# Kernel tuning notes

Measured on AMD Instinct MI355X. Metric: run time of the kernel, lower is better.

Reference implementation:

```python
import jax, jax.numpy as jnp
import numpy as np

N_NODES = 100_000
N_EDGES = 3_200_000
D_IN, D_EDGE, D_HID, D_OUT = 8, 4, 32, 16
NEG_SLOPE = 0.2  # PyG GATv2Conv default


def setup_inputs() -> dict:
    key = jax.random.key(0)
    ks = jax.random.split(key, 13)
    s = 0.1
    return {
        "x": jax.random.normal(ks[0], (N_NODES, D_IN), jnp.float32),
        "edge_index": jax.random.randint(ks[1], (2, N_EDGES), 0, N_NODES, dtype=jnp.int64),
        "edge_attr": jax.random.normal(ks[2], (N_EDGES, D_EDGE), jnp.float32),
        "Wl1": jax.random.normal(ks[3], (D_IN, D_HID), jnp.float32) * s,
        "Wr1": jax.random.normal(ks[4], (D_IN, D_HID), jnp.float32) * s,
        "We1": jax.random.normal(ks[5], (D_EDGE, D_HID), jnp.float32) * s,
        "att1": jax.random.normal(ks[6], (D_HID,), jnp.float32) * s,
        "b1": jnp.zeros((D_HID,), jnp.float32),
        "Wl2": jax.random.normal(ks[7], (D_HID, D_OUT), jnp.float32) * s,
        "Wr2": jax.random.normal(ks[8], (D_HID, D_OUT), jnp.float32) * s,
        "We2": jax.random.normal(ks[9], (D_EDGE, D_OUT), jnp.float32) * s,
        "att2": jax.random.normal(ks[10], (D_OUT,), jnp.float32) * s,
        "b2": jnp.zeros((D_OUT,), jnp.float32),
    }


def _segment_softmax(score, seg, n):
    m = jax.ops.segment_max(score, seg, num_segments=n)
    e = jnp.exp(score - m[seg])
    z = jax.ops.segment_sum(e, seg, num_segments=n)
    return e / z[seg]


def _gatv2(x, src, dst, ea_raw, Wl, Wr, We, att, bias, n):
    # GATv2 (heads=1): score_ij = att . leaky_relu(Wl x_j + Wr x_i + We e_ij)
    xl = x @ Wl            # [N, d]
    xr = x @ Wr            # [N, d]
    ea = ea_raw @ We       # [E, d]
    h = jax.nn.leaky_relu(xl[src] + xr[dst] + ea, NEG_SLOPE)  # [E, d]
    score = h @ att        # [E]
    alpha = _segment_softmax(score, dst, n)
    out = jax.ops.segment_sum(alpha[:, None] * xl[src], dst, num_segments=n)
    return out + bias


def reference(x, edge_index, edge_attr, Wl1, Wr1, We1, att1, b1, Wl2, Wr2, We2, att2, b2):
    n = x.shape[0]
    src, dst = edge_index[0], edge_index[1]
    # add_self_loops=True with fill_value='mean': self-loop edge_attr = mean of
    # incoming raw edge_attr per target node (0 for isolated targets)
    ones = jnp.ones((src.shape[0],), x.dtype)
    cnt = jax.ops.segment_sum(ones, dst, num_segments=n)
    loop_attr = jax.ops.segment_sum(edge_attr, dst, num_segments=n) / jnp.maximum(cnt, 1.0)[:, None]
    ar = jnp.arange(n, dtype=src.dtype)
    src2 = jnp.concatenate([src, ar])
    dst2 = jnp.concatenate([dst, ar])
    ea2 = jnp.concatenate([edge_attr, loop_attr], axis=0)
    h = jax.nn.relu(_gatv2(x, src2, dst2, ea2, Wl1, Wr1, We1, att1, b1, n))
    out = _gatv2(h, src2, dst2, ea2, Wl2, Wr2, We2, att2, b2, n)
    return out.reshape(-1)
```

## Files before the change

kernel.cpp:

```cpp
#include <hip/hip_runtime.h>

#define NEG_SLOPE 0.2f
#define CHUNK 4096
#define KMAX  512
#define NBLKMAX 1024
#define CAPB  9472

__global__ __launch_bounds__(1024) void k_bin(const int* __restrict__ ei,
                                              const float* __restrict__ eattr,
                                              int* __restrict__ cloff,
                                              int* __restrict__ ssrc,
                                              float4* __restrict__ seat,
                                              int E, int K) {
    __shared__ int s_off[KMAX + 1];
    __shared__ int s_scan[1024];
    __shared__ int s_ssrc[CHUNK];
    __shared__ float4 s_seat[CHUNK];
    int t = threadIdx.x;
    for (int i = t; i <= K; i += 1024) s_off[i] = 0;
    __syncthreads();
    int base = blockIdx.x * CHUNK;
    int Ec = min(CHUNK, E - base);
    unsigned pack[CHUNK / 1024];
#pragma unroll
    for (int i = 0; i < CHUNK / 1024; i++) {
        int el = t + 1024 * i;
        pack[i] = 0xFFFFFFFFu;
        if (el < Ec) {
            int dst = ei[E + base + el];
            int b = dst >> 8;
            int r = atomicAdd(&s_off[b], 1);
            pack[i] = ((unsigned)b << 20) | ((unsigned)(dst & 255) << 12) | (unsigned)r;
        }
    }
    __syncthreads();
    int x0 = (t <= K) ? s_off[t] : 0;
    s_scan[t] = x0;
    __syncthreads();
    for (int off = 1; off < 1024; off <<= 1) {
        int y = (t >= off) ? s_scan[t - off] : 0;
        __syncthreads();
        s_scan[t] += y;
        __syncthreads();
    }
    if (t <= K) s_off[t] = s_scan[t] - x0;
    __syncthreads();
#pragma unroll
    for (int i = 0; i < CHUNK / 1024; i++) {
        int el = t + 1024 * i;
        if (el < Ec) {
            unsigned p = pack[i];
            int b = p >> 20;
            int dl = (p >> 12) & 255;
            int r = p & 0xFFF;
            int pos = s_off[b] + r;
            int e = base + el;
            s_ssrc[pos] = ei[e] | (dl << 17);
            s_seat[pos] = *(const float4*)(eattr + 4ll * e);
        }
    }
    __syncthreads();
    for (int pos = t; pos < Ec; pos += 1024) {
        ssrc[base + pos] = s_ssrc[pos];
        seat[base + pos] = s_seat[pos];
    }
    for (int i = t; i <= K; i += 1024)
        cloff[(long long)blockIdx.x * (K + 1) + i] = s_off[i];
}

__global__ void k_transp(const int* __restrict__ in, int* __restrict__ out, int R, int C) {
    __shared__ int tile[32][33];
    int c0 = blockIdx.x * 32, r0 = blockIdx.y * 32;
    int c = c0 + threadIdx.x, r = r0 + threadIdx.y;
    if (r < R && c < C) tile[threadIdx.y][threadIdx.x] = in[(long long)r * C + c];
    __syncthreads();
    int oc = r0 + threadIdx.x, orr = c0 + threadIdx.y;
    if (orr < C && oc < R) out[(long long)orr * R + oc] = tile[threadIdx.x][threadIdx.y];
}

__global__ void k_btot(const int* __restrict__ cloffT, int* __restrict__ bucketTotal,
                       int K, int NBLK) {
    int b = (blockIdx.x * blockDim.x + threadIdx.x) >> 6;
    int lane = threadIdx.x & 63;
    if (b >= K) return;
    const int* r0 = cloffT + (long long)b * NBLK;
    const int* r1 = r0 + NBLK;
    int s = 0;
    for (int c = lane; c < NBLK; c += 64) s += r1[c] - r0[c];
#pragma unroll
    for (int off = 32; off >= 1; off >>= 1) s += __shfl_xor(s, off, 64);
    if (lane == 0) bucketTotal[b] = s;
}

__global__ void k_scanK(const int* __restrict__ bucketTotal, int* __restrict__ slotBase,
                        int* __restrict__ qofs, int N, int K) {
    __shared__ int s[512];
    int t = threadIdx.x;
    int v[4];
    int sum = 0;
    int base = t * 4;
    for (int j = 0; j < 4; j++) {
        int b = base + j, x = 0;
        if (b < K) { int nb = min(256, N - (b << 8)); x = bucketTotal[b] + nb; }
        v[j] = sum;
        sum += x;
    }
    s[t] = sum;
    __syncthreads();
    for (int off = 1; off < 512; off <<= 1) {
        int x = (t >= off) ? s[t - off] : 0;
        __syncthreads();
        s[t] += x;
        __syncthreads();
    }
    int tb = s[t] - sum;
    for (int j = 0; j < 4; j++) {
        int b = base + j;
        if (b < K) slotBase[b] = tb + v[j];
    }
    if (t == 511) { slotBase[K] = s[511]; qofs[4ll * N] = s[511]; }
}

__global__ __launch_bounds__(1024, 2) void k_perm(const int* __restrict__ ssrc,
                                                  const float4* __restrict__ seat,
                                                  const int* __restrict__ cloffT,
                                                  const int* __restrict__ slotBase,
                                                  int* __restrict__ qofs,
                                                  int* __restrict__ fsrc,
                                                  float4* __restrict__ feat,
                                                  int N, int K, int NBLK, int QDIV) {
    __shared__ int co[NBLKMAX], qq[NBLKMAX + 1], sc[NBLKMAX];
    __shared__ int hist2[1024], cur2[1024], lst2[1024], sc2[1024];
    __shared__ int hist[256];
    __shared__ float lsum[256][4];
    __shared__ int s_inv[CAPB];
    int b = blockIdx.x, t = threadIdx.x;
    int nb = min(256, N - (b << 8));
    hist2[t] = 0; cur2[t] = 0;
    if (t < 256) { lsum[t][0] = 0.f; lsum[t][1] = 0.f; lsum[t][2] = 0.f; lsum[t][3] = 0.f; }
    const int* r0 = cloffT + (long long)b * NBLK;
    const int* r1 = r0 + NBLK;
    int len = 0;
    if (t < NBLK) { int c0v = r0[t]; len = r1[t] - c0v; co[t] = c0v; }
    sc[t] = (t < NBLK) ? len : 0;
    __syncthreads();
    for (int off = 1; off < NBLKMAX; off <<= 1) {
        int x = (t >= off) ? sc[t - off] : 0;
        __syncthreads();
        sc[t] += x;
        __syncthreads();
    }
    if (t < NBLK) qq[t] = sc[t] - len;
    if (t == NBLKMAX - 1) qq[NBLK] = sc[NBLKMAX - 1];
    __syncthreads();
    int Eb = qq[NBLK];
    for (int i = t; i < Eb; i += 1024) {
        int lo2 = 0, hi2 = NBLK;
        while (lo2 + 1 < hi2) { int mid = (lo2 + hi2) >> 1; if (qq[mid] <= i) lo2 = mid; else hi2 = mid; }
        int g = lo2 * CHUNK + co[lo2] + (i - qq[lo2]);
        int p = ssrc[g];
        int q = (int)((unsigned)(p & 0x1FFFF) / (unsigned)QDIV);
        atomicAdd(&hist2[(((p >> 17) & 255) << 2) | q], 1);
    }
    __syncthreads();
    if (t < 256) {
        int c = hist2[4 * t] + hist2[4 * t + 1] + hist2[4 * t + 2] + hist2[4 * t + 3];
        hist[t] = c;
        if (t < nb) {
            int node = (b << 8) + t;
            int qs = (int)((unsigned)node / (unsigned)QDIV);
            hist2[4 * t + qs] += 1;
            cur2[4 * t + qs] = 1;
        }
    }
    __syncthreads();
    sc2[t] = hist2[t];
    __syncthreads();
    for (int off = 1; off < 1024; off <<= 1) {
        int x = (t >= off) ? sc2[t - off] : 0;
        __syncthreads();
        sc2[t] += x;
        __syncthreads();
    }
    lst2[t] = sc2[t] - hist2[t];
    __syncthreads();
    int lo = slotBase[b];
    if (t < 4 * nb) qofs[((long long)b << 10) + t] = lo + lst2[t];
    if (t < nb) {
        int node = (b << 8) + t;
        int qs = (int)((unsigned)node / (unsigned)QDIV);
        s_inv[lst2[4 * t + qs]] = -(t + 1);
    }
    __syncthreads();
    for (int i = t; i < Eb; i += 1024) {
        int lo2 = 0, hi2 = NBLK;
        while (lo2 + 1 < hi2) { int mid = (lo2 + hi2) >> 1; if (qq[mid] <= i) lo2 = mid; else hi2 = mid; }
        int g = lo2 * CHUNK + co[lo2] + (i - qq[lo2]);
        int p = ssrc[g];
        int q = (int)((unsigned)(p & 0x1FFFF) / (unsigned)QDIV);
        int bin = (((p >> 17) & 255) << 2) | q;
        int r = atomicAdd(&cur2[bin], 1);
        s_inv[lst2[bin] + r] = g;
    }
    __syncthreads();
    int tot = Eb + nb;
    int pos = t;
    for (; pos + 1024 < tot; pos += 2048) {
        int gA = s_inv[pos];
        int gB = s_inv[pos + 1024];
        bool vA = gA >= 0, vB = gB >= 0;
        int cA = vA ? gA : 0, cB = vB ? gB : 0;
        int pA = ssrc[cA];
        int pB = ssrc[cB];
        float4 aA = seat[cA];
        float4 aB = seat[cB];
        if (vA) {
            long long gp = lo + pos;
            fsrc[gp] = pA & 0x1FFFF;
            feat[gp] = aA;
            int dl = (pA >> 17) & 255;
            atomicAdd(&lsum[dl][0], aA.x); atomicAdd(&lsum[dl][1], aA.y);
            atomicAdd(&lsum[dl][2], aA.z); atomicAdd(&lsum[dl][3], aA.w);
        }
        if (vB) {
            long long gp = lo + pos + 1024;
            fsrc[gp] = pB & 0x1FFFF;
            feat[gp] = aB;
            int dl = (pB >> 17) & 255;
            atomicAdd(&lsum[dl][0], aB.x); atomicAdd(&lsum[dl][1], aB.y);
            atomicAdd(&lsum[dl][2], aB.z); atomicAdd(&lsum[dl][3], aB.w);
        }
    }
    for (; pos < tot; pos += 1024) {
        int g = s_inv[pos];
        if (g >= 0) {
            int p = ssrc[g];
            float4 a = seat[g];
            long long gp = lo + pos;
            fsrc[gp] = p & 0x1FFFF;
            feat[gp] = a;
            int dl = (p >> 17) & 255;
            atomicAdd(&lsum[dl][0], a.x); atomicAdd(&lsum[dl][1], a.y);
            atomicAdd(&lsum[dl][2], a.z); atomicAdd(&lsum[dl][3], a.w);
        }
    }
    __syncthreads();
    if (t < nb) {
        int node = (b << 8) + t;
        int qs = (int)((unsigned)node / (unsigned)QDIV);
        float inv = 1.f / fmaxf((float)hist[t], 1.f);
        long long pos2 = lo + lst2[4 * t + qs];
        fsrc[pos2] = node;
        feat[pos2] = make_float4(lsum[t][0] * inv, lsum[t][1] * inv,
                                 lsum[t][2] * inv, lsum[t][3] * inv);
    }
}

template <int DIN, int D>
__global__ void k_xform(const float* __restrict__ x, const float* __restrict__ Wl,
                        const float* __restrict__ Wr, float* __restrict__ xl,
                        float* __restrict__ xr, int N) {
    __shared__ float sWl[DIN * D], sWr[DIN * D];
    for (int i = threadIdx.x; i < DIN * D; i += blockDim.x) { sWl[i] = Wl[i]; sWr[i] = Wr[i]; }
    __syncthreads();
    int t = blockIdx.x * blockDim.x + threadIdx.x;
    if (t >= N * D) return;
    int n = t / D, d = t % D;
    const float* xp = x + (long long)n * DIN;
    float sl = 0.f, sr = 0.f;
#pragma unroll
    for (int k = 0; k < DIN; k++) {
        float xv = xp[k];
        sl += xv * sWl[k * D + d];
        sr += xv * sWr[k * D + d];
    }
    xl[t] = sl;
    xr[t] = sr;
}

template <int L>
__device__ __forceinline__ void gat_edge(bool valid, const float4& a, const float4& xlv,
                                         const float4& we0, const float4& we1,
                                         const float4& we2, const float4& we3,
                                         const float4& av, const float4& xrv,
                                         float4& acc, float& z) {
    float4 v;
    v.x = fmaf(a.x, we0.x, xrv.x); v.x = fmaf(a.y, we1.x, v.x);
    v.x = fmaf(a.z, we2.x, v.x);   v.x = fmaf(a.w, we3.x, v.x); v.x += xlv.x;
    v.y = fmaf(a.x, we0.y, xrv.y); v.y = fmaf(a.y, we1.y, v.y);
    v.y = fmaf(a.z, we2.y, v.y);   v.y = fmaf(a.w, we3.y, v.y); v.y += xlv.y;
    v.z = fmaf(a.x, we0.z, xrv.z); v.z = fmaf(a.y, we1.z, v.z);
    v.z = fmaf(a.z, we2.z, v.z);   v.z = fmaf(a.w, we3.z, v.z); v.z += xlv.z;
    v.w = fmaf(a.x, we0.w, xrv.w); v.w = fmaf(a.y, we1.w, v.w);
    v.w = fmaf(a.z, we2.w, v.w);   v.w = fmaf(a.w, we3.w, v.w); v.w += xlv.w;
    v.x = v.x > 0.f ? v.x : NEG_SLOPE * v.x;
    v.y = v.y > 0.f ? v.y : NEG_SLOPE * v.y;
    v.z = v.z > 0.f ? v.z : NEG_SLOPE * v.z;
    v.w = v.w > 0.f ? v.w : NEG_SLOPE * v.w;
    float sc = av.x * v.x + av.y * v.y + av.z * v.z + av.w * v.w;
#pragma unroll
    for (int off = L / 2; off >= 1; off >>= 1) sc += __shfl_xor(sc, off, 64);
    float ev = valid ? __expf(sc) : 0.f;
    z += ev;
    acc.x = fmaf(ev, xlv.x, acc.x);
    acc.y = fmaf(ev, xlv.y, acc.y);
    acc.z = fmaf(ev, xlv.z, acc.z);
    acc.w = fmaf(ev, xlv.w, acc.w);
}

template <int D, bool RELU>
__global__ void k_gat(const int* __restrict__ fsrc,
                      const float4* __restrict__ feat,
                      const int* __restrict__ qofs,
                      const float* __restrict__ xl, const float* __restrict__ xr,
                      const float* __restrict__ We, const float* __restrict__ att,
                      const float* __restrict__ bias, float* __restrict__ out, int N) {
    constexpr int L = D / 4;
    constexpr int G = 64 / L;
    int w = (blockIdx.x * blockDim.x + threadIdx.x) >> 6;
    int lane = threadIdx.x & 63;
    if (w >= N) return;
    int g = lane / L;
    int j = lane % L;
    int s0 = qofs[4 * w], s1 = qofs[4 * w + 4];
    int cnt = s1 - s0;

    const float4 we0 = *(const float4*)(We + 0 * D + 4 * j);
    const float4 we1 = *(const float4*)(We + 1 * D + 4 * j);
    const float4 we2 = *(const float4*)(We + 2 * D + 4 * j);
    const float4 we3 = *(const float4*)(We + 3 * D + 4 * j);
    const float4 av  = *(const float4*)(att + 4 * j);
    const float4 xrv = *(const float4*)(xr + (long long)w * D + 4 * j);

    float4 acc = make_float4(0.f, 0.f, 0.f, 0.f);
    float z = 0.f;

    int it = 0;
    for (; (it + 2) * G <= cnt; it += 2) {
        int sl = s0 + it * G + g;
        int srcA = fsrc[sl];
        int srcB = fsrc[sl + G];
        float4 aA = feat[sl];
        float4 aB = feat[sl + G];
        float4 xA = *(const float4*)(xl + (long long)srcA * D + 4 * j);
        float4 xB = *(const float4*)(xl + (long long)srcB * D + 4 * j);
        gat_edge<L>(true, aA, xA, we0, we1, we2, we3, av, xrv, acc, z);
        gat_edge<L>(true, aB, xB, we0, we1, we2, we3, av, xrv, acc, z);
    }
    for (; it * G < cnt; ++it) {
        int o = it * G + g;
        bool v = o < cnt;
        int sl = s0 + min(o, cnt - 1);
        int src = fsrc[sl];
        float4 a = feat[sl];
        float4 xv = *(const float4*)(xl + (long long)src * D + 4 * j);
        gat_edge<L>(v, a, xv, we0, we1, we2, we3, av, xrv, acc, z);
    }

#pragma unroll
    for (int off = 32; off >= L; off >>= 1) {
        acc.x += __shfl_xor(acc.x, off, 64);
        acc.y += __shfl_xor(acc.y, off, 64);
        acc.z += __shfl_xor(acc.z, off, 64);
        acc.w += __shfl_xor(acc.w, off, 64);
        z += __shfl_xor(z, off, 64);
    }

    if (g == 0) {
        float inv = 1.0f / z;
        float4 bv = *(const float4*)(bias + 4 * j);
        float4 o;
        o.x = acc.x * inv + bv.x;
        o.y = acc.y * inv + bv.y;
        o.z = acc.z * inv + bv.z;
        o.w = acc.w * inv + bv.w;
        if (RELU) {
            o.x = fmaxf(o.x, 0.f); o.y = fmaxf(o.y, 0.f);
            o.z = fmaxf(o.z, 0.f); o.w = fmaxf(o.w, 0.f);
        }
        *(float4*)(out + (long long)w * D + 4 * j) = o;
    }
}

extern "C" void kernel_launch(void* const* d_in, const int* in_sizes, int n_in,
                              void* d_out, int out_size, void* d_ws, size_t ws_size,
                              hipStream_t stream) {
    const float* x     = (const float*)d_in[0];
    const int*   ei    = (const int*)d_in[1];
    const float* eattr = (const float*)d_in[2];
    const float* Wl1   = (const float*)d_in[3];
    const float* Wr1   = (const float*)d_in[4];
    const float* We1   = (const float*)d_in[5];
    const float* att1  = (const float*)d_in[6];
    const float* b1    = (const float*)d_in[7];
    const float* Wl2   = (const float*)d_in[8];
    const float* Wr2   = (const float*)d_in[9];
    const float* We2   = (const float*)d_in[10];
    const float* att2  = (const float*)d_in[11];
    const float* b2    = (const float*)d_in[12];

    const int N = in_sizes[0] / 8;
    const int E = in_sizes[1] / 2;
    const int K = (N + 255) >> 8;
    const int NBLK = (E + CHUNK - 1) / CHUNK;
    const int QDIV = (N + 3) / 4;

    int* iws = (int*)d_ws;
    size_t o = 0;
    int* bucketTotal = iws + o; o += K;
    int* slotBase    = iws + o; o += K + 1;
    int* qofs        = iws + o; o += 4ll * N + 1;
    int* cloff       = iws + o; o += (size_t)NBLK * (K + 1);
    int* cloffT      = iws + o; o += (size_t)(K + 1) * NBLK;
    o = (o + 7) & ~(size_t)7;
    int*    fsrc = (int*)(iws + o);    o += (size_t)(E + N);
    o = (o + 3) & ~(size_t)3;
    float4* feat = (float4*)(iws + o); o += 4ll * (E + N);
    size_t stage = o;
    int*    ssrc = (int*)(iws + o);    o += (size_t)E;
    o = (o + 3) & ~(size_t)3;
    float4* seat = (float4*)(iws + o); o += 4ll * E;
    float* xl = (float*)(iws + stage);
    float* xr = xl + 32ll * N;
    float* h  = xr + 32ll * N;

    const int B = 256;
    auto cdiv = [](long long a, long long b) { return (int)((a + b - 1) / b); };

    k_bin<<<NBLK, 1024, 0, stream>>>(ei, eattr, cloff, ssrc, seat, E, K);
    dim3 tb(32, 32);
    k_transp<<<dim3(cdiv(K + 1, 32), cdiv(NBLK, 32)), tb, 0, stream>>>(cloff, cloffT, NBLK, K + 1);
    k_btot<<<cdiv(64ll * K, B), B, 0, stream>>>(cloffT, bucketTotal, K, NBLK);
    k_scanK<<<1, 512, 0, stream>>>(bucketTotal, slotBase, qofs, N, K);
    k_perm<<<K, 1024, 0, stream>>>(ssrc, seat, cloffT, slotBase, qofs, fsrc, feat, N, K, NBLK, QDIV);

    k_xform<8, 32><<<cdiv(32ll * N, B), B, 0, stream>>>(x, Wl1, Wr1, xl, xr, N);
    k_gat<32, true><<<cdiv(N, 4), B, 0, stream>>>(fsrc, feat, qofs, xl, xr, We1, att1, b1, h, N);

    k_xform<32, 16><<<cdiv(16ll * N, B), B, 0, stream>>>(h, Wl2, Wr2, xl, xr, N);
    k_gat<16, false><<<cdiv(N, 4), B, 0, stream>>>(fsrc, feat, qofs, xl, xr, We2, att2, b2, (float*)d_out, N);
}
```

Baseline: 490.4 us.

## Use 128-node dst buckets, drop source-quadrant sub-sort, cache packed edges in LDS

Halves the destination bucket size from 256 to 128 nodes, which doubles the number of k_perm blocks and shrinks each block's shared-memory footprint. The per-destination 4-way source-quadrant sub-sort is removed, so the CSR uses a single start offset per node instead of four, and the 1024-wide histogram scan becomes a 128-wide one. The packed src/dst word and the global index are now kept in LDS, so the scatter pass no longer re-reads ssrc from global memory. The cost is that edges within a node are no longer grouped by source range, which may reduce gather locality for xl in the GAT kernels.

```diff
diff --git a/kernel.cpp b/kernel.cpp
--- a/kernel.cpp
+++ b/kernel.cpp
@@ -2,9 +2,9 @@
 
 #define NEG_SLOPE 0.2f
 #define CHUNK 4096
-#define KMAX  512
+#define KMAX  1024
 #define NBLKMAX 1024
-#define CAPB  9472
+#define CAPB  4864
 
 __global__ __launch_bounds__(1024) void k_bin(const int* __restrict__ ei,
                                               const float* __restrict__ eattr,
@@ -28,9 +28,9 @@
         pack[i] = 0xFFFFFFFFu;
         if (el < Ec) {
             int dst = ei[E + base + el];
-            int b = dst >> 8;
+            int b = dst >> 7;
             int r = atomicAdd(&s_off[b], 1);
-            pack[i] = ((unsigned)b << 20) | ((unsigned)(dst & 255) << 12) | (unsigned)r;
+            pack[i] = ((unsigned)b << 19) | ((unsigned)(dst & 127) << 12) | (unsigned)r;
         }
     }
     __syncthreads();
@@ -50,8 +50,8 @@
         int el = t + 1024 * i;
         if (el < Ec) {
             unsigned p = pack[i];
-            int b = p >> 20;
-            int dl = (p >> 12) & 255;
+            int b = p >> 19;
+            int dl = (p >> 12) & 127;
             int r = p & 0xFFF;
             int pos = s_off[b] + r;
             int e = base + el;
@@ -93,7 +93,7 @@
 }
 
 __global__ void k_scanK(const int* __restrict__ bucketTotal, int* __restrict__ slotBase,
-                        int* __restrict__ qofs, int N, int K) {
+                        int* __restrict__ start, int N, int K) {
     __shared__ int s[512];
     int t = threadIdx.x;
     int v[4];
@@ -101,7 +101,7 @@
     int base = t * 4;
     for (int j = 0; j < 4; j++) {
         int b = base + j, x = 0;
-        if (b < K) { int nb = min(256, N - (b << 8)); x = bucketTotal[b] + nb; }
+        if (b < K) { int nb = min(128, N - (b << 7)); x = bucketTotal[b] + nb; }
         v[j] = sum;
         sum += x;
     }
@@ -118,26 +118,28 @@
         int b = base + j;
         if (b < K) slotBase[b] = tb + v[j];
     }
-    if (t == 511) { slotBase[K] = s[511]; qofs[4ll * N] = s[511]; }
+    if (t == 511) { slotBase[K] = s[511]; start[N] = s[511]; }
 }
 
 __global__ __launch_bounds__(1024, 2) void k_perm(const int* __restrict__ ssrc,
                                                   const float4* __restrict__ seat,
                                                   const int* __restrict__ cloffT,
                                                   const int* __restrict__ slotBase,
-                                                  int* __restrict__ qofs,
+                                                  int* __restrict__ start,
                                                   int* __restrict__ fsrc,
                                                   float4* __restrict__ feat,
-                                                  int N, int K, int NBLK, int QDIV) {
+                                                  int N, int K, int NBLK) {
     __shared__ int co[NBLKMAX], qq[NBLKMAX + 1], sc[NBLKMAX];
-    __shared__ int hist2[1024], cur2[1024], lst2[1024], sc2[1024];
-    __shared__ int hist[256];
-    __shared__ float lsum[256][4];
-    __shared__ int s_inv[CAPB];
+    __shared__ int histE[128], cur[128], lst[128];
+    __shared__ float lsum[128][4];
+    __shared__ int s_op[CAPB];
+    __shared__ int s_og[CAPB];
     int b = blockIdx.x, t = threadIdx.x;
-    int nb = min(256, N - (b << 8));
-    hist2[t] = 0; cur2[t] = 0;
-    if (t < 256) { lsum[t][0] = 0.f; lsum[t][1] = 0.f; lsum[t][2] = 0.f; lsum[t][3] = 0.f; }
+    int nb = min(128, N - (b << 7));
+    if (t < 128) {
+        histE[t] = 0;
+        lsum[t][0] = 0.f; lsum[t][1] = 0.f; lsum[t][2] = 0.f; lsum[t][3] = 0.f;
+    }
     const int* r0 = cloffT + (long long)b * NBLK;
     const int* r1 = r0 + NBLK;
     int len = 0;
@@ -159,37 +161,29 @@
         while (lo2 + 1 < hi2) { int mid = (lo2 + hi2) >> 1; if (qq[mid] <= i) lo2 = mid; else hi2 = mid; }
         int g = lo2 * CHUNK + co[lo2] + (i - qq[lo2]);
         int p = ssrc[g];
-        int q = (int)((unsigned)(p & 0x1FFFF) / (unsigned)QDIV);
-        atomicAdd(&hist2[(((p >> 17) & 255) << 2) | q], 1);
-    }
-    __syncthreads();
-    if (t < 256) {
-        int c = hist2[4 * t] + hist2[4 * t + 1] + hist2[4 * t + 2] + hist2[4 * t + 3];
-        hist[t] = c;
-        if (t < nb) {
-            int node = (b << 8) + t;
-            int qs = (int)((unsigned)node / (unsigned)QDIV);
-            hist2[4 * t + qs] += 1;
-            cur2[4 * t + qs] = 1;
-        }
-    }
-    __syncthreads();
-    sc2[t] = hist2[t];
-    __syncthreads();
-    for (int off = 1; off < 1024; off <<= 1) {
-        int x = (t >= off) ? sc2[t - off] : 0;
-        __syncthreads();
-        sc2[t] += x;
-        __syncthreads();
-    }
-    lst2[t] = sc2[t] - hist2[t];
+        atomicAdd(&histE[(p >> 17) & 127], 1);
+    }
+    __syncthreads();
+    int cnt = 0;
+    if (t < 128) {
+        cnt = (t < nb) ? histE[t] + 1 : 0;
+        lst[t] = cnt;
+        cur[t] = (t < nb) ? 1 : 0;
+    }
+    __syncthreads();
+    for (int off = 1; off < 128; off <<= 1) {
+        int x = 0;
+        if (t < 128 && t >= off) x = lst[t - off];
+        __syncthreads();
+        if (t < 128) lst[t] += x;
+        __syncthreads();
+    }
+    if (t < 128) lst[t] -= cnt;
     __syncthreads();
     int lo = slotBase[b];
-    if (t < 4 * nb) qofs[((long long)b << 10) + t] = lo + lst2[t];
     if (t < nb) {
-        int node = (b << 8) + t;
-        int qs = (int)((unsigned)node / (unsigned)QDIV);
-        s_inv[lst2[4 * t + qs]] = -(t + 1);
+        start[(b << 7) + t] = lo + lst[t];
+        s_op[lst[t]] = -1;
     }
     __syncthreads();
     for (int i = t; i < Eb; i += 1024) {
@@ -197,28 +191,28 @@
         while (lo2 + 1 < hi2) { int mid = (lo2 + hi2) >> 1; if (qq[mid] <= i) lo2 = mid; else hi2 = mid; }
         int g = lo2 * CHUNK + co[lo2] + (i - qq[lo2]);
         int p = ssrc[g];
-        int q = (int)((unsigned)(p & 0x1FFFF) / (unsigned)QDIV);
-        int bin = (((p >> 17) & 255) << 2) | q;
-        int r = atomicAdd(&cur2[bin], 1);
-        s_inv[lst2[bin] + r] = g;
+        int dl = (p >> 17) & 127;
+        int r = atomicAdd(&cur[dl], 1);
+        int op = lst[dl] + r;
+        s_op[op] = p;
+        s_og[op] = g;
     }
     __syncthreads();
     int tot = Eb + nb;
     int pos = t;
     for (; pos + 1024 < tot; pos += 2048) {
-        int gA = s_inv[pos];
-        int gB = s_inv[pos + 1024];
-        bool vA = gA >= 0, vB = gB >= 0;
-        int cA = vA ? gA : 0, cB = vB ? gB : 0;
-        int pA = ssrc[cA];
-        int pB = ssrc[cB];
-        float4 aA = seat[cA];
-        float4 aB = seat[cB];
+        int pA = s_op[pos];
+        int pB = s_op[pos + 1024];
+        int gA = s_og[pos];
+        int gB = s_og[pos + 1024];
+        bool vA = pA >= 0, vB = pB >= 0;
+        float4 aA = seat[vA ? gA : 0];
+        float4 aB = seat[vB ? gB : 0];
         if (vA) {
             long long gp = lo + pos;
             fsrc[gp] = pA & 0x1FFFF;
             feat[gp] = aA;
-            int dl = (pA >> 17) & 255;
+            int dl = (pA >> 17) & 127;
             atomicAdd(&lsum[dl][0], aA.x); atomicAdd(&lsum[dl][1], aA.y);
             atomicAdd(&lsum[dl][2], aA.z); atomicAdd(&lsum[dl][3], aA.w);
         }
@@ -226,33 +220,32 @@
             long long gp = lo + pos + 1024;
             fsrc[gp] = pB & 0x1FFFF;
             feat[gp] = aB;
-            int dl = (pB >> 17) & 255;
+            int dl = (pB >> 17) & 127;
             atomicAdd(&lsum[dl][0], aB.x); atomicAdd(&lsum[dl][1], aB.y);
             atomicAdd(&lsum[dl][2], aB.z); atomicAdd(&lsum[dl][3], aB.w);
         }
     }
     for (; pos < tot; pos += 1024) {
-        int g = s_inv[pos];
-        if (g >= 0) {
-            int p = ssrc[g];
+        int p = s_op[pos];
+        if (p >= 0) {
+            int g = s_og[pos];
             float4 a = seat[g];
             long long gp = lo + pos;
             fsrc[gp] = p & 0x1FFFF;
             feat[gp] = a;
-            int dl = (p >> 17) & 255;
+            int dl = (p >> 17) & 127;
             atomicAdd(&lsum[dl][0], a.x); atomicAdd(&lsum[dl][1], a.y);
             atomicAdd(&lsum[dl][2], a.z); atomicAdd(&lsum[dl][3], a.w);
         }
     }
     __syncthreads();
     if (t < nb) {
-        int node = (b << 8) + t;
-        int qs = (int)((unsigned)node / (unsigned)QDIV);
-        float inv = 1.f / fmaxf((float)hist[t], 1.f);
-        long long pos2 = lo + lst2[4 * t + qs];
-        fsrc[pos2] = node;
-        feat[pos2] = make_float4(lsum[t][0] * inv, lsum[t][1] * inv,
-                                 lsum[t][2] * inv, lsum[t][3] * inv);
+        int node = (b << 7) + t;
+        float inv = 1.f / fmaxf((float)histE[t], 1.f);
+        long long pp = lo + lst[t];
+        fsrc[pp] = node;
+        feat[pp] = make_float4(lsum[t][0] * inv, lsum[t][1] * inv,
+                               lsum[t][2] * inv, lsum[t][3] * inv);
     }
 }
 
@@ -311,7 +304,7 @@
 template <int D, bool RELU>
 __global__ void k_gat(const int* __restrict__ fsrc,
                       const float4* __restrict__ feat,
-                      const int* __restrict__ qofs,
+                      const int* __restrict__ start,
                       const float* __restrict__ xl, const float* __restrict__ xr,
                       const float* __restrict__ We, const float* __restrict__ att,
                       const float* __restrict__ bias, float* __restrict__ out, int N) {
@@ -322,7 +315,7 @@
     if (w >= N) return;
     int g = lane / L;
     int j = lane % L;
-    int s0 = qofs[4 * w], s1 = qofs[4 * w + 4];
+    int s0 = start[w], s1 = start[w + 1];
     int cnt = s1 - s0;
 
     const float4 we0 = *(const float4*)(We + 0 * D + 4 * j);
@@ -401,15 +394,14 @@
 
     const int N = in_sizes[0] / 8;
     const int E = in_sizes[1] / 2;
-    const int K = (N + 255) >> 8;
+    const int K = (N + 127) >> 7;
     const int NBLK = (E + CHUNK - 1) / CHUNK;
-    const int QDIV = (N + 3) / 4;
 
     int* iws = (int*)d_ws;
     size_t o = 0;
     int* bucketTotal = iws + o; o += K;
     int* slotBase    = iws + o; o += K + 1;
-    int* qofs        = iws + o; o += 4ll * N + 1;
+    int* start       = iws + o; o += N + 1;
     int* cloff       = iws + o; o += (size_t)NBLK * (K + 1);
     int* cloffT      = iws + o; o += (size_t)(K + 1) * NBLK;
     o = (o + 7) & ~(size_t)7;
@@ -431,12 +423,12 @@
     dim3 tb(32, 32);
     k_transp<<<dim3(cdiv(K + 1, 32), cdiv(NBLK, 32)), tb, 0, stream>>>(cloff, cloffT, NBLK, K + 1);
     k_btot<<<cdiv(64ll * K, B), B, 0, stream>>>(cloffT, bucketTotal, K, NBLK);
-    k_scanK<<<1, 512, 0, stream>>>(bucketTotal, slotBase, qofs, N, K);
-    k_perm<<<K, 1024, 0, stream>>>(ssrc, seat, cloffT, slotBase, qofs, fsrc, feat, N, K, NBLK, QDIV);
+    k_scanK<<<1, 512, 0, stream>>>(bucketTotal, slotBase, start, N, K);
+    k_perm<<<K, 1024, 0, stream>>>(ssrc, seat, cloffT, slotBase, start, fsrc, feat, N, K, NBLK);
 
     k_xform<8, 32><<<cdiv(32ll * N, B), B, 0, stream>>>(x, Wl1, Wr1, xl, xr, N);
-    k_gat<32, true><<<cdiv(N, 4), B, 0, stream>>>(fsrc, feat, qofs, xl, xr, We1, att1, b1, h, N);
+    k_gat<32, true><<<cdiv(N, 4), B, 0, stream>>>(fsrc, feat, start, xl, xr, We1, att1, b1, h, N);
 
     k_xform<32, 16><<<cdiv(16ll * N, B), B, 0, stream>>>(h, Wl2, Wr2, xl, xr, N);
-    k_gat<16, false><<<cdiv(N, 4), B, 0, stream>>>(fsrc, feat, qofs, xl, xr, We2, att2, b2, (float*)d_out, N);
-}
+    k_gat<16, false><<<cdiv(N, 4), B, 0, stream>>>(fsrc, feat, start, xl, xr, We2, att2, b2, (float*)d_out, N);
+}
```

Result: no change. 498.2 us (+1.6%).
